# Kernel tuning notes

Measured on AMD Instinct MI355X. Metric: run time of the kernel, lower is better.

## Reference

```python
import jax, jax.numpy as jnp
import numpy as np

DIM = 16        # lagrangian.dim -> y has 2*DIM phase-space coords
HID = 128       # hidden width of the parametric Lagrangian
BATCH = 32768


def setup_inputs() -> dict:
    key = jax.random.key(0)
    k1, k2, k3, k4 = jax.random.split(key, 4)
    y = jax.random.normal(k1, (BATCH, 2 * DIM), dtype=jnp.float32)
    # small-scale init keeps J_{qdot,qdot} = I + (MLP Hessian block) well conditioned
    W1 = jax.random.normal(k2, (HID, 2 * DIM), dtype=jnp.float32) * (1.0 / np.sqrt(2 * DIM))
    b1 = jax.random.normal(k3, (HID,), dtype=jnp.float32) * 0.1
    w2 = jax.random.normal(k4, (HID,), dtype=jnp.float32) * 0.1
    return {"y": y, "W1": W1, "b1": b1, "w2": w2}


def _lagrangian(y_vec, W1, b1, w2):
    """Scalar Lagrangian L(q, qdot) for a single phase-space vector y_vec [2*DIM]."""
    qdot = y_vec[DIM:]
    kinetic = 0.5 * jnp.dot(qdot, qdot)
    return kinetic + jnp.dot(w2, jnp.tanh(W1 @ y_vec + b1))


def reference(y, W1, b1, w2):
    """Acceleration qdotdot = (dL/dq - qdot . J_{q,qdot}) . J_{qdot,qdot}^{-1}.

    Instead of the original O(dim^2) repeated tf.gradients calls, compute the
    full gradient and Hessian once per sample via fused forward-over-reverse
    autodiff, vmapped over the batch.
    """
    d = DIM
    L = lambda yv: _lagrangian(yv, W1, b1, w2)
    grad_fn = jax.grad(L)
    hess_fn = jax.jacfwd(grad_fn)  # forward-over-reverse Hessian, one sweep

    g = jax.vmap(grad_fn)(y)   # [B, 2d]   full dL/dy
    H = jax.vmap(hess_fn)(y)   # [B, 2d, 2d]  full Hessian d2L/(dy dy)

    qdot = y[:, d:]            # [B, d]
    dLdq = g[:, :d]            # [B, d]
    J_qqdot = H[:, :d, d:]     # [B, d, d]  d2L/(dq_i dqdot_j)
    J_qdqd_inv = jnp.linalg.inv(H[:, d:, d:])  # [B, d, d]

    rhs = dLdq - jnp.einsum('bi,bij->bj', qdot, J_qqdot)
    qdotdot = jnp.einsum('bi,bij->bj', rhs, J_qdqd_inv)
    return qdotdot
```

## Files before the change

### kernel.cpp

```cpp
#include <hip/hip_runtime.h>
#include <math.h>

#define DIMQ 16
#define HID  128
#define SPB  32
#define NTHREADS 256

typedef __attribute__((ext_vector_type(8))) _Float16 f16x8;
typedef __attribute__((ext_vector_type(4))) _Float16 f16x4;
typedef __attribute__((ext_vector_type(4))) float f32x4;
typedef __attribute__((ext_vector_type(2))) float v2f;

#define OFF_WFF  0
#define OFF_ABT  8192
#define OFF_USP  16384
#define OFF_SST  32768
#define OFF_MSCR 0
#define LDS_BYTES 40960

__device__ __forceinline__ int axor(int row, int off) { return off ^ ((row & 7) << 3); }
__device__ __forceinline__ int mswz(int s, int off) {
    return s * 320 + (off ^ ((s & 7) << 2));
}
__device__ __forceinline__ f16x8 pack8(float4 a, float4 b) {
    f16x8 r;
    r[0]=(_Float16)a.x; r[1]=(_Float16)a.y; r[2]=(_Float16)a.z; r[3]=(_Float16)a.w;
    r[4]=(_Float16)b.x; r[5]=(_Float16)b.y; r[6]=(_Float16)b.z; r[7]=(_Float16)b.w;
    return r;
}

__global__ __launch_bounds__(NTHREADS, 4)
void lag_accel_kernel(const float* __restrict__ y,
                      const float* __restrict__ W1,
                      const float* __restrict__ b1,
                      const float* __restrict__ w2,
                      float* __restrict__ out)
{
    __shared__ __align__(16) char smem[LDS_BYTES];
    _Float16* Wff = (_Float16*)(smem + OFF_WFF);
    _Float16* ABT = (_Float16*)(smem + OFF_ABT);
    _Float16* usp = (_Float16*)(smem + OFF_USP);
    _Float16* sst = (_Float16*)(smem + OFF_SST);

    const int tid = threadIdx.x;
    const long long s0 = (long long)blockIdx.x * SPB;

    const int wave = tid >> 6;
    const int lane = tid & 63;
    const int grp  = lane >> 4;
    const int j    = lane & 15;

    f16x8 yf[2];
#pragma unroll
    for (int st = 0; st < 2; ++st) {
        const float4* yg = (const float4*)(y + (s0 + st * 16 + j) * 32 + (grp << 3));
        yf[st] = pack8(yg[0], yg[1]);
    }

#pragma unroll
    for (int it = 0; it < 2; ++it) {
        const int slot = tid + it * 256;
        const int ht_ = slot >> 6, grp_ = (slot >> 4) & 3, j_ = slot & 15;
        const float4* src = (const float4*)(W1 + (ht_ * 16 + j_) * 32 + (grp_ << 3));
        *(f16x8*)&Wff[slot * 8] = pack8(src[0], src[1]);
    }
#pragma unroll
    for (int it = 0; it < 2; ++it) {
        const int idx = tid + it * 256;
        const int k = idx & 31, h0 = (idx >> 5) << 3;
        float v[8];
#pragma unroll
        for (int i = 0; i < 8; ++i) v[i] = W1[(h0 + i) * 32 + k];
        f16x8 p;
#pragma unroll
        for (int i = 0; i < 8; ++i) p[i] = (_Float16)v[i];
        const int j_ = (k < 16) ? k : (k - 16);
        const int off = (k < 16) ? h0 : (128 + h0);
        *(f16x8*)&ABT[(j_ << 8) + axor(j_, off)] = p;
    }

    __syncthreads();

    f32x4 zacc[2][2], aacc[2][2];
    float4 w2v[2];
#pragma unroll
    for (int t = 0; t < 2; ++t) {
        const int ht = wave * 2 + t;
        f16x8 aW  = *(const f16x8*)&Wff[((ht * 4 + grp) * 16 + j) * 8];
        f16x8 aAl = *(const f16x8*)&Wff[((ht * 4 + (grp & 1)) * 16 + j) * 8];
        f16x8 aA;
#pragma unroll
        for (int e = 0; e < 8; ++e) aA[e] = (grp >= 2) ? aAl[e] : (_Float16)0.0f;
        float4 b1v = *(const float4*)&b1[ht * 16 + (grp << 2)];
        w2v[t] = *(const float4*)&w2[ht * 16 + (grp << 2)];
        f32x4 ci; ci[0] = b1v.x; ci[1] = b1v.y; ci[2] = b1v.z; ci[3] = b1v.w;
        f32x4 zf = {0.0f, 0.0f, 0.0f, 0.0f};
#pragma unroll
        for (int st = 0; st < 2; ++st) {
            zacc[t][st] = __builtin_amdgcn_mfma_f32_16x16x32_f16(aW, yf[st], ci, 0, 0, 0);
            aacc[t][st] = __builtin_amdgcn_mfma_f32_16x16x32_f16(aA, yf[st], zf, 0, 0, 0);
        }
    }

#define EWST(t, st)                                                      \
    {                                                                    \
        const int h4 = (wave * 2 + (t)) * 16 + (grp << 2);               \
        const int smp2 = (st) * 16 + j;                                  \
        _Float16 su[4], sn[4], sv[4];                                    \
        _Pragma("unroll")                                                \
        for (int r = 0; r < 4; ++r) {                                    \
            float z  = zacc[t][st][r], aq = aacc[t][st][r];              \
            float w2c = (r == 0) ? w2v[t].x : (r == 1) ? w2v[t].y         \
                       : (r == 2) ? w2v[t].z : w2v[t].w;                 \
            float e  = __expf(2.0f * z);                                 \
            float rr = 2.0f * __builtin_amdgcn_rcpf(e + 1.0f);           \
            float t_ = 1.0f - rr;                                        \
            float u  = w2c * (rr * (2.0f - rr));                         \
            float s  = -2.0f * t_ * u;                                   \
            float sp = s * aq;                                           \
            su[r] = (_Float16)u; sn[r] = (_Float16)(-sp);                \
            sv[r] = (_Float16)s;                                         \
        }                                                                \
        f16x4 pa = {su[0], su[1], su[2], su[3]};                         \
        f16x4 pb = {sn[0], sn[1], sn[2], sn[3]};                         \
        f16x4 pc = {sv[0], sv[1], sv[2], sv[3]};                         \
        *(f16x4*)&usp[(smp2 << 8) + axor(smp2, h4)]       = pa;          \
        *(f16x4*)&usp[(smp2 << 8) + axor(smp2, 128 + h4)] = pb;          \
        *(f16x4*)&sst[(smp2 << 7) + axor(smp2, h4)]       = pc;          \
    }
    EWST(0, 0) EWST(0, 1) EWST(1, 0) EWST(1, 1)
#undef EWST

    __syncthreads();

    f32x4 racc = {0.0f, 0.0f, 0.0f, 0.0f};
    if (wave < 2) {
#pragma unroll
        for (int kc = 0; kc < 8; ++kc) {
            const int o = (kc << 5) + (grp << 3);
            const int smp = wave * 16 + j;
            f16x8 af = *(const f16x8*)&ABT[(j << 8) + axor(j, o)];
            f16x8 bf = *(const f16x8*)&usp[(smp << 8) + axor(smp, o)];
            racc = __builtin_amdgcn_mfma_f32_16x16x32_f16(af, bf, racc, 0, 0, 0);
        }
    }

    f32x4 acc[8];
    {
        f32x4 ident;
#pragma unroll
        for (int r = 0; r < 4; ++r) ident[r] = ((grp << 2) + r == j) ? 1.0f : 0.0f;
#pragma unroll
        for (int gs = 0; gs < 8; ++gs) acc[gs] = ident;
    }
#pragma unroll
    for (int kc = 0; kc < 4; ++kc) {
        const int o = (kc << 5) + (grp << 3);
        f16x8 bfrag = *(const f16x8*)&ABT[(j << 8) + axor(j, 128 + o)];
#pragma unroll
        for (int gs = 0; gs < 8; ++gs) {
            const int smp = wave * 8 + gs;
            f16x8 sfrag = *(const f16x8*)&sst[(smp << 7) + axor(smp, o)];
            f16x8 afrag = sfrag * bfrag;
            acc[gs] = __builtin_amdgcn_mfma_f32_16x16x32_f16(afrag, bfrag, acc[gs], 0, 0, 0);
        }
    }

    __syncthreads();

    float* Mscr = (float*)(smem + OFF_MSCR);
#pragma unroll
    for (int gs = 0; gs < 8; ++gs) {
        float4 v;
        v.x = acc[gs][0]; v.y = acc[gs][1]; v.z = acc[gs][2]; v.w = acc[gs][3];
        *(float4*)&Mscr[mswz(wave * 8 + gs, j * 20 + (grp << 2))] = v;
    }

    __syncthreads();

    if (wave >= 2) return;
    const int sl = lane & 15;
    const int rb = lane >> 4;
    const int s  = wave * 16 + sl;

    v2f M2[4][8];
    float r4[4], d4[4];
#pragma unroll
    for (int r = 0; r < 4; ++r) {
        const int ro = (4 * rb + r) * 20;
        float4 v0 = *(const float4*)&Mscr[mswz(s, ro + 0)];
        float4 v1 = *(const float4*)&Mscr[mswz(s, ro + 4)];
        float4 v2 = *(const float4*)&Mscr[mswz(s, ro + 8)];
        float4 v3 = *(const float4*)&Mscr[mswz(s, ro + 12)];
        M2[r][0] = (v2f){v0.x, v0.y}; M2[r][1] = (v2f){v0.z, v0.w};
        M2[r][2] = (v2f){v1.x, v1.y}; M2[r][3] = (v2f){v1.z, v1.w};
        M2[r][4] = (v2f){v2.x, v2.y}; M2[r][5] = (v2f){v2.z, v2.w};
        M2[r][6] = (v2f){v3.x, v3.y}; M2[r][7] = (v2f){v3.z, v3.w};
        r4[r] = racc[r];
        d4[r] = 1.0f;
    }

#pragma unroll
    for (int k = 0; k < 16; ++k) {
        const int src = sl + ((k >> 2) << 4);
        float piv = __shfl(M2[k & 3][k >> 1][k & 1], src, 64);
        float rk  = __shfl(r4[k & 3], src, 64);
        float invp = __builtin_amdgcn_rcpf(piv);
        invp = invp * (2.0f - piv * invp);
        float f[4];
#pragma unroll
        for (int r = 0; r < 4; ++r) {
            float fr = M2[r][k >> 1][k & 1] * invp;
            const bool isk = ((rb << 2) + r) == k;
            f[r]  = isk ? 0.0f : fr;
            d4[r] = isk ? piv : d4[r];
            r4[r] = fmaf(-f[r], rk, r4[r]);
        }
        const int i2s = (k >> 1) + (k & 1);
#pragma unroll
        for (int i2 = i2s; i2 < 8; ++i2) {
            float p0 = (2 * i2 == k) ? piv : __shfl(M2[k & 3][i2][0], src, 64);
            float p1 = __shfl(M2[k & 3][i2][1], src, 64);
            v2f pv = {p0, p1};
#pragma unroll
            for (int r = 0; r < 4; ++r) {
                v2f fv = {-f[r], -f[r]};
                M2[r][i2] = __builtin_elementwise_fma(fv, pv, M2[r][i2]);
            }
        }
    }

    float4 xo;
    {
        float i0 = __builtin_amdgcn_rcpf(d4[0]); i0 = i0 * (2.0f - d4[0] * i0);
        float i1 = __builtin_amdgcn_rcpf(d4[1]); i1 = i1 * (2.0f - d4[1] * i1);
        float i2 = __builtin_amdgcn_rcpf(d4[2]); i2 = i2 * (2.0f - d4[2] * i2);
        float i3 = __builtin_amdgcn_rcpf(d4[3]); i3 = i3 * (2.0f - d4[3] * i3);
        xo.x = r4[0] * i0; xo.y = r4[1] * i1; xo.z = r4[2] * i2; xo.w = r4[3] * i3;
    }
    *(float4*)&out[(s0 + s) * DIMQ + (rb << 2)] = xo;
}

extern "C" void kernel_launch(void* const* d_in, const int* in_sizes, int n_in,
                              void* d_out, int out_size, void* d_ws, size_t ws_size,
                              hipStream_t stream) {
    const float* y  = (const float*)d_in[0];
    const float* W1 = (const float*)d_in[1];
    const float* b1 = (const float*)d_in[2];
    const float* w2 = (const float*)d_in[3];
    float* out = (float*)d_out;
    const int batch = in_sizes[0] / 32;
    const int blocks = (batch + SPB - 1) / SPB;
    lag_accel_kernel<<<blocks, NTHREADS, 0, stream>>>(y, W1, b1, w2, out);
}
```

Baseline: 19.57 us.

## Double samples per block to 64 with 512 threads, one hidden tile per wave

Raises samples per block from 32 to 64 and threads from 256 to 512, so each of 8 waves owns one 16-wide hidden tile across four sample subtiles instead of two tiles across two. The per-block W1 staging into LDS is now amortized over twice as many samples, and twice as many waves do the final solve. LDS doubles to 80 KB, which limits blocks per CU, and the grid halves. Launch bounds still say 4 blocks of 512 threads, which may force register pressure.

```diff
diff --git a/kernel.cpp b/kernel.cpp
--- a/kernel.cpp
+++ b/kernel.cpp
@@ -3,8 +3,8 @@
 
 #define DIMQ 16
 #define HID  128
-#define SPB  32
-#define NTHREADS 256
+#define SPB  64
+#define NTHREADS 512
 
 typedef __attribute__((ext_vector_type(8))) _Float16 f16x8;
 typedef __attribute__((ext_vector_type(4))) _Float16 f16x4;
@@ -14,9 +14,9 @@
 #define OFF_WFF  0
 #define OFF_ABT  8192
 #define OFF_USP  16384
-#define OFF_SST  32768
+#define OFF_SST  49152
 #define OFF_MSCR 0
-#define LDS_BYTES 40960
+#define LDS_BYTES 81920
 
 __device__ __forceinline__ int axor(int row, int off) { return off ^ ((row & 7) << 3); }
 __device__ __forceinline__ int mswz(int s, int off) {
@@ -49,25 +49,22 @@
     const int lane = tid & 63;
     const int grp  = lane >> 4;
     const int j    = lane & 15;
-
-    f16x8 yf[2];
-#pragma unroll
-    for (int st = 0; st < 2; ++st) {
+    const int ht   = wave;
+
+    f16x8 yf[4];
+#pragma unroll
+    for (int st = 0; st < 4; ++st) {
         const float4* yg = (const float4*)(y + (s0 + st * 16 + j) * 32 + (grp << 3));
         yf[st] = pack8(yg[0], yg[1]);
     }
 
-#pragma unroll
-    for (int it = 0; it < 2; ++it) {
-        const int slot = tid + it * 256;
-        const int ht_ = slot >> 6, grp_ = (slot >> 4) & 3, j_ = slot & 15;
+    {
+        const int ht_ = tid >> 6, grp_ = (tid >> 4) & 3, j_ = tid & 15;
         const float4* src = (const float4*)(W1 + (ht_ * 16 + j_) * 32 + (grp_ << 3));
-        *(f16x8*)&Wff[slot * 8] = pack8(src[0], src[1]);
-    }
-#pragma unroll
-    for (int it = 0; it < 2; ++it) {
-        const int idx = tid + it * 256;
-        const int k = idx & 31, h0 = (idx >> 5) << 3;
+        *(f16x8*)&Wff[tid * 8] = pack8(src[0], src[1]);
+    }
+    {
+        const int k = tid & 31, h0 = (tid >> 5) << 3;
         float v[8];
 #pragma unroll
         for (int i = 0; i < 8; ++i) v[i] = W1[(h0 + i) * 32 + k];
@@ -81,64 +78,53 @@
 
     __syncthreads();
 
-    f32x4 zacc[2][2], aacc[2][2];
-    float4 w2v[2];
-#pragma unroll
-    for (int t = 0; t < 2; ++t) {
-        const int ht = wave * 2 + t;
-        f16x8 aW  = *(const f16x8*)&Wff[((ht * 4 + grp) * 16 + j) * 8];
-        f16x8 aAl = *(const f16x8*)&Wff[((ht * 4 + (grp & 1)) * 16 + j) * 8];
-        f16x8 aA;
-#pragma unroll
-        for (int e = 0; e < 8; ++e) aA[e] = (grp >= 2) ? aAl[e] : (_Float16)0.0f;
-        float4 b1v = *(const float4*)&b1[ht * 16 + (grp << 2)];
-        w2v[t] = *(const float4*)&w2[ht * 16 + (grp << 2)];
-        f32x4 ci; ci[0] = b1v.x; ci[1] = b1v.y; ci[2] = b1v.z; ci[3] = b1v.w;
-        f32x4 zf = {0.0f, 0.0f, 0.0f, 0.0f};
-#pragma unroll
-        for (int st = 0; st < 2; ++st) {
-            zacc[t][st] = __builtin_amdgcn_mfma_f32_16x16x32_f16(aW, yf[st], ci, 0, 0, 0);
-            aacc[t][st] = __builtin_amdgcn_mfma_f32_16x16x32_f16(aA, yf[st], zf, 0, 0, 0);
-        }
-    }
-
-#define EWST(t, st)                                                      \
-    {                                                                    \
-        const int h4 = (wave * 2 + (t)) * 16 + (grp << 2);               \
-        const int smp2 = (st) * 16 + j;                                  \
-        _Float16 su[4], sn[4], sv[4];                                    \
-        _Pragma("unroll")                                                \
-        for (int r = 0; r < 4; ++r) {                                    \
-            float z  = zacc[t][st][r], aq = aacc[t][st][r];              \
-            float w2c = (r == 0) ? w2v[t].x : (r == 1) ? w2v[t].y         \
-                       : (r == 2) ? w2v[t].z : w2v[t].w;                 \
-            float e  = __expf(2.0f * z);                                 \
-            float rr = 2.0f * __builtin_amdgcn_rcpf(e + 1.0f);           \
-            float t_ = 1.0f - rr;                                        \
-            float u  = w2c * (rr * (2.0f - rr));                         \
-            float s  = -2.0f * t_ * u;                                   \
-            float sp = s * aq;                                           \
-            su[r] = (_Float16)u; sn[r] = (_Float16)(-sp);                \
-            sv[r] = (_Float16)s;                                         \
-        }                                                                \
-        f16x4 pa = {su[0], su[1], su[2], su[3]};                         \
-        f16x4 pb = {sn[0], sn[1], sn[2], sn[3]};                         \
-        f16x4 pc = {sv[0], sv[1], sv[2], sv[3]};                         \
-        *(f16x4*)&usp[(smp2 << 8) + axor(smp2, h4)]       = pa;          \
-        *(f16x4*)&usp[(smp2 << 8) + axor(smp2, 128 + h4)] = pb;          \
-        *(f16x4*)&sst[(smp2 << 7) + axor(smp2, h4)]       = pc;          \
-    }
-    EWST(0, 0) EWST(0, 1) EWST(1, 0) EWST(1, 1)
-#undef EWST
+    f16x8 aW  = *(const f16x8*)&Wff[((ht * 4 + grp) * 16 + j) * 8];
+    f16x8 aAl = *(const f16x8*)&Wff[((ht * 4 + (grp & 1)) * 16 + j) * 8];
+    f16x8 aA;
+#pragma unroll
+    for (int e = 0; e < 8; ++e) aA[e] = (grp >= 2) ? aAl[e] : (_Float16)0.0f;
+    float4 b1v = *(const float4*)&b1[ht * 16 + (grp << 2)];
+    float4 w2v = *(const float4*)&w2[ht * 16 + (grp << 2)];
+    f32x4 ci; ci[0] = b1v.x; ci[1] = b1v.y; ci[2] = b1v.z; ci[3] = b1v.w;
+    const f32x4 zf = {0.0f, 0.0f, 0.0f, 0.0f};
+    const int h4 = ht * 16 + (grp << 2);
+
+#pragma unroll
+    for (int st = 0; st < 4; ++st) {
+        f32x4 zacc = __builtin_amdgcn_mfma_f32_16x16x32_f16(aW, yf[st], ci, 0, 0, 0);
+        f32x4 aacc = __builtin_amdgcn_mfma_f32_16x16x32_f16(aA, yf[st], zf, 0, 0, 0);
+        const int smp2 = st * 16 + j;
+        _Float16 su[4], sn[4], sv[4];
+#pragma unroll
+        for (int r = 0; r < 4; ++r) {
+            float z  = zacc[r], aq = aacc[r];
+            float w2c = (r == 0) ? w2v.x : (r == 1) ? w2v.y
+                       : (r == 2) ? w2v.z : w2v.w;
+            float e  = __expf(2.0f * z);
+            float rr = 2.0f * __builtin_amdgcn_rcpf(e + 1.0f);
+            float t_ = 1.0f - rr;
+            float u  = w2c * (rr * (2.0f - rr));
+            float s  = -2.0f * t_ * u;
+            float sp = s * aq;
+            su[r] = (_Float16)u; sn[r] = (_Float16)(-sp);
+            sv[r] = (_Float16)s;
+        }
+        f16x4 pa = {su[0], su[1], su[2], su[3]};
+        f16x4 pb = {sn[0], sn[1], sn[2], sn[3]};
+        f16x4 pc = {sv[0], sv[1], sv[2], sv[3]};
+        *(f16x4*)&usp[(smp2 << 8) + axor(smp2, h4)]       = pa;
+        *(f16x4*)&usp[(smp2 << 8) + axor(smp2, 128 + h4)] = pb;
+        *(f16x4*)&sst[(smp2 << 7) + axor(smp2, h4)]       = pc;
+    }
 
     __syncthreads();
 
     f32x4 racc = {0.0f, 0.0f, 0.0f, 0.0f};
-    if (wave < 2) {
+    if (wave < 4) {
+        const int smp = wave * 16 + j;
 #pragma unroll
         for (int kc = 0; kc < 8; ++kc) {
             const int o = (kc << 5) + (grp << 3);
-            const int smp = wave * 16 + j;
             f16x8 af = *(const f16x8*)&ABT[(j << 8) + axor(j, o)];
             f16x8 bf = *(const f16x8*)&usp[(smp << 8) + axor(smp, o)];
             racc = __builtin_amdgcn_mfma_f32_16x16x32_f16(af, bf, racc, 0, 0, 0);
@@ -178,7 +164,7 @@
 
     __syncthreads();
 
-    if (wave >= 2) return;
+    if (wave >= 4) return;
     const int sl = lane & 15;
     const int rb = lane >> 4;
     const int s  = wave * 16 + sl;
```

After: 18.95 us (median of 2 runs). -3.2%, faster.
